# Performance work log

Hardware: AMD Instinct MI355X
Metric: run time of the kernel (lower is better)

Reference implementation:

```python
import jax, jax.numpy as jnp
import numpy as np
import math

B, S, D = 16, 1024, 512

def setup_inputs() -> dict:
    key = jax.random.key(0)
    ks = jax.random.split(key, 7)
    s = 1.0 / math.sqrt(D)
    return {
        "features_4h": jax.random.normal(ks[0], (B, S, D), jnp.float32),
        "features_1d": jax.random.normal(ks[1], (B, S, D), jnp.float32),
        "features_1w": jax.random.normal(ks[2], (B, S, D), jnp.float32),
        "Wq": jax.random.normal(ks[3], (D, D), jnp.float32) * s,
        "bq": jnp.zeros((D,), jnp.float32),
        "Wk": jax.random.normal(ks[4], (D, D), jnp.float32) * s,
        "bk": jnp.zeros((D,), jnp.float32),
        "Wv": jax.random.normal(ks[5], (D, D), jnp.float32) * s,
        "bv": jnp.zeros((D,), jnp.float32),
        "tf_weights": jnp.ones((3,), jnp.float32),
    }

def reference(features_4h, features_1d, features_1w, Wq, bq, Wk, bk, Wv, bv, tf_weights):
    # stacked: [B, T=3, S, D]
    stacked = jnp.stack([features_4h, features_1d, features_1w], axis=1)
    scale = 1.0 / math.sqrt(stacked.shape[-1])
    # torch nn.Linear: x @ W.T + b
    Q = jnp.einsum("btsd,ed->btse", stacked, Wq) + bq
    K = jnp.einsum("btsd,ed->btse", stacked, Wk) + bk
    V = jnp.einsum("btsd,ed->btse", stacked, Wv) + bv
    scores = jnp.einsum("btqd,btkd->btqk", Q, K) * scale  # [B,T,S,S]
    attn = jax.nn.softmax(scores, axis=-1)
    attended = jnp.einsum("btqk,btkd->btqd", attn, V)  # [B,T,S,D]
    w = jax.nn.softmax(tf_weights, axis=0)  # [T]
    return jnp.einsum("btsd,t->bsd", attended, w)  # [B,S,D]
```

## Files before the change

### kernel.cpp

```cpp
#include <hip/hip_runtime.h>
#include <cstdint>

typedef __bf16 bf16x8 __attribute__((ext_vector_type(8)));
typedef unsigned short u16x8 __attribute__((ext_vector_type(8)));
typedef float f32x4 __attribute__((ext_vector_type(4)));


__device__ __forceinline__ unsigned short f2bf(float x){
  unsigned u = __float_as_uint(x);
  u += 0x7fffu + ((u >> 16) & 1u);
  return (unsigned short)(u >> 16);
}

__device__ __forceinline__ void gload16(const void* src, void* dst){
  auto g = reinterpret_cast<const uint32_t __attribute__((address_space(1)))*>(
             reinterpret_cast<uintptr_t>(src));
  auto l = reinterpret_cast<uint32_t __attribute__((address_space(3)))*>(
             reinterpret_cast<uintptr_t>(dst));
  __builtin_amdgcn_global_load_lds(g, l, 16, 0, 0);
}

__device__ __forceinline__ void stage_tile(const unsigned short* __restrict__ g, size_t ld,
                                           unsigned short* l, int tid){
  #pragma unroll
  for (int i = 0; i < 4; ++i){
    int j = i * 256 + tid;
    int r = j >> 3, cc = j & 7;
    int c = cc ^ (r & 7);
    gload16(g + (size_t)r * ld + c * 8, l + (size_t)(i * 256 + (tid & 192)) * 8);
  }
}

__device__ __forceinline__ bf16x8 frag_at(const unsigned short* l, int row, int kch){
  int ch = kch ^ (row & 7);
  return *(const bf16x8*)(l + (row << 6) + (ch << 3));
}

__global__ void k_w1(const float* __restrict__ Wk, const float* __restrict__ bq,
                     float* __restrict__ w1){
  __shared__ float red[4][64];
  int d = blockIdx.x * 64 + (threadIdx.x & 63);
  int eq = threadIdx.x >> 6;
  float s = 0.f;
  #pragma unroll 8
  for (int e = eq * 128; e < eq * 128 + 128; ++e) s += Wk[(size_t)e * 512 + d] * bq[e];
  red[eq][threadIdx.x & 63] = s;
  __syncthreads();
  if (eq == 0)
    w1[d] = (red[0][threadIdx.x] + red[1][threadIdx.x] + red[2][threadIdx.x] +
             red[3][threadIdx.x]) * 0.04419417382415922f;
}

__global__ void k_conv_wt(const float* __restrict__ Wq, const float* __restrict__ Wk,
                          unsigned short* __restrict__ WqT, unsigned short* __restrict__ WkT){
  __shared__ float tl[64][65];
  int bi = blockIdx.x;
  const float* src = (bi & 64) ? Wk : Wq;
  unsigned short* dst = (bi & 64) ? WkT : WqT;
  int te = (bi >> 3) & 7, td = bi & 7;
  int tid = threadIdx.x;
  #pragma unroll
  for (int i = 0; i < 4; ++i){
    int q = i * 256 + tid;
    int r = q >> 4, c4 = q & 15;
    f32x4 v = *(const f32x4*)(src + (size_t)(te * 64 + r) * 512 + td * 64 + c4 * 4);
    tl[r][c4 * 4 + 0] = v[0]; tl[r][c4 * 4 + 1] = v[1];
    tl[r][c4 * 4 + 2] = v[2]; tl[r][c4 * 4 + 3] = v[3];
  }
  __syncthreads();
  #pragma unroll
  for (int i = 0; i < 2; ++i){
    int q = i * 256 + tid;
    int r = q >> 3, c8 = q & 7;
    u16x8 o;
    #pragma unroll
    for (int j = 0; j < 8; ++j) o[j] = f2bf(tl[c8 * 8 + j][r]);
    *(u16x8*)(dst + (size_t)(td * 64 + r) * 512 + te * 64 + c8 * 8) = o;
  }
}

__global__ void k_conv_wv(const float* __restrict__ Wv, unsigned short* __restrict__ out){
  size_t e = ((size_t)blockIdx.x * 256 + threadIdx.x) * 8;
  f32x4 v0 = *(const f32x4*)(Wv + e), v1 = *(const f32x4*)(Wv + e + 4);
  u16x8 o;
  o[0] = f2bf(v0[0]); o[1] = f2bf(v0[1]); o[2] = f2bf(v0[2]); o[3] = f2bf(v0[3]);
  o[4] = f2bf(v1[0]); o[5] = f2bf(v1[1]); o[6] = f2bf(v1[2]); o[7] = f2bf(v1[3]);
  *(u16x8*)(out + e) = o;
}

__global__ void k_conv_feat(const float* __restrict__ f0, const float* __restrict__ f1,
                            const float* __restrict__ f2, const float* __restrict__ w1,
                            unsigned short* __restrict__ Xb, float* __restrict__ vcol){
  size_t i = (size_t)blockIdx.x * blockDim.x + threadIdx.x;
  size_t e = i * 8;
  size_t bt = e >> 19;
  size_t rest = e & ((1u << 19) - 1);
  int b = (int)(bt / 3), t = (int)(bt % 3);
  const float* src = (t == 0 ? f0 : (t == 1 ? f1 : f2)) + ((size_t)b << 19) + rest;
  f32x4 v0 = *(const f32x4*)(src);
  f32x4 v1 = *(const f32x4*)(src + 4);
  u16x8 o;
  o[0] = f2bf(v0[0]); o[1] = f2bf(v0[1]); o[2] = f2bf(v0[2]); o[3] = f2bf(v0[3]);
  o[4] = f2bf(v1[0]); o[5] = f2bf(v1[1]); o[6] = f2bf(v1[2]); o[7] = f2bf(v1[3]);
  *(u16x8*)(Xb + e) = o;
  int l = threadIdx.x & 63;
  f32x4 wa = *(const f32x4*)(w1 + l * 8);
  f32x4 wb = *(const f32x4*)(w1 + l * 8 + 4);
  float p = v0[0]*wa[0] + v0[1]*wa[1] + v0[2]*wa[2] + v0[3]*wa[3]
          + v1[0]*wb[0] + v1[1]*wb[1] + v1[2]*wb[2] + v1[3]*wb[3];
  p += __shfl_xor(p, 1);  p += __shfl_xor(p, 2);  p += __shfl_xor(p, 4);
  p += __shfl_xor(p, 8);  p += __shfl_xor(p, 16); p += __shfl_xor(p, 32);
  if (l == 0) vcol[i >> 6] = p;
}

template<int MODE>
__global__ __launch_bounds__(256, 2)
void k_gemm_proj(const unsigned short* __restrict__ A, const unsigned short* __restrict__ Bm,
                 const float* __restrict__ bias, unsigned short* __restrict__ C, int N, float scale){
  __shared__ __align__(16) unsigned short Al[2][8192];
  __shared__ __align__(16) unsigned short Bl[2][8192];
  const int tid = threadIdx.x;
  const int l  = tid & 63;
  const int wid = tid >> 6;
  const int lr = l & 15;
  const int lg = l >> 4;
  const int cpx = gridDim.x >> 3;
  const int wg = (blockIdx.x & 7) * cpx + (blockIdx.x >> 3);
  const int nbc = N >> 7;
  int rb, cb;
  if (MODE == 1){ cb = wg >> 2; rb = wg & 3; }
  else          { rb = wg / nbc; cb = wg % nbc; }
  const unsigned short* Ab = A + (size_t)rb * 128 * 512;
  const unsigned short* Bb = Bm + (size_t)cb * 128 * 512;

  const f32x4 zero4 = {0.f, 0.f, 0.f, 0.f};
  f32x4 acc[4][4];
  #pragma unroll
  for (int i = 0; i < 4; ++i)
    #pragma unroll
    for (int j = 0; j < 4; ++j) acc[i][j] = zero4;

  stage_tile(Ab, 512, &Al[0][0], tid);
  stage_tile(Bb, 512, &Bl[0][0], tid);
  __syncthreads();

  const int wr = wid >> 1, wc = wid & 1;

  for (int kb = 0; kb < 8; ++kb){
    const int cur = kb & 1;
    if (kb < 7){
      stage_tile(Ab + (kb + 1) * 64, 512, &Al[cur ^ 1][0], tid);
      stage_tile(Bb + (kb + 1) * 64, 512, &Bl[cur ^ 1][0], tid);
    }
    #pragma unroll
    for (int ks = 0; ks < 2; ++ks){
      bf16x8 af[4], bf[4];
      #pragma unroll
      for (int i = 0; i < 4; ++i) af[i] = frag_at(&Al[cur][0], wr * 64 + i * 16 + lr, ks * 4 + lg);
      #pragma unroll
      for (int j = 0; j < 4; ++j) bf[j] = frag_at(&Bl[cur][0], wc * 64 + j * 16 + lr, ks * 4 + lg);
      #pragma unroll
      for (int i = 0; i < 4; ++i)
        #pragma unroll
        for (int j = 0; j < 4; ++j)
          acc[i][j] = __builtin_amdgcn_mfma_f32_16x16x32_bf16(af[i], bf[j], acc[i][j], 0, 0, 0);
    }
    __syncthreads();
  }

  #pragma unroll
  for (int j = 0; j < 4; ++j){
    int col = cb * 128 + wc * 64 + j * 16 + lr;
    float bc = (MODE == 0 && bias) ? bias[col] : 0.f;
    #pragma unroll
    for (int i = 0; i < 4; ++i){
      int row0 = rb * 128 + wr * 64 + i * 16 + lg * 4;
      #pragma unroll
      for (int r = 0; r < 4; ++r){
        int row = row0 + r;
        float v = (acc[i][j][r] + ((MODE == 0) ? bc : bias[row])) * scale;
        size_t addr;
        if (MODE == 0) addr = (size_t)row * N + col;
        else           addr = ((size_t)(col >> 10) << 19) + ((size_t)row << 10) + (size_t)(col & 1023);
        C[addr] = f2bf(v);
      }
    }
  }
}

__global__ __launch_bounds__(256, 2)
void k_gemm_qk(const unsigned short* __restrict__ Gb, const unsigned short* __restrict__ Xb,
               unsigned short* __restrict__ S, int bt0){
  __shared__ __align__(16) unsigned short Al[2][8192];
  __shared__ __align__(16) unsigned short Bl[2][8192];
  const int tid = threadIdx.x;
  const int l  = tid & 63;
  const int wid = tid >> 6;
  const int lr = l & 15;
  const int lg = l >> 4;
  const int cpx = gridDim.x >> 3;
  const int wg = (blockIdx.x & 7) * cpx + (blockIdx.x >> 3);
  const int btl = wg >> 6;
  const int bt = bt0 + btl;
  const int tile = wg & 63;
  const int rb = tile >> 3, cb = tile & 7;
  const unsigned short* Ab = Gb + ((size_t)bt << 19) + (size_t)rb * 128 * 512;
  const unsigned short* Bb = Xb + ((size_t)bt << 19) + (size_t)cb * 128 * 512;
  unsigned short* Cb = S + ((size_t)btl << 20);

  const f32x4 zero4 = {0.f, 0.f, 0.f, 0.f};
  f32x4 acc[4][4];
  #pragma unroll
  for (int i = 0; i < 4; ++i)
    #pragma unroll
    for (int j = 0; j < 4; ++j) acc[i][j] = zero4;

  stage_tile(Ab, 512, &Al[0][0], tid);
  stage_tile(Bb, 512, &Bl[0][0], tid);
  __syncthreads();

  const int wr = wid >> 1, wc = wid & 1;

  for (int kb = 0; kb < 8; ++kb){
    const int cur = kb & 1;
    if (kb < 7){
      stage_tile(Ab + (kb + 1) * 64, 512, &Al[cur ^ 1][0], tid);
      stage_tile(Bb + (kb + 1) * 64, 512, &Bl[cur ^ 1][0], tid);
    }
    #pragma unroll
    for (int ks = 0; ks < 2; ++ks){
      bf16x8 af[4], bf[4];
      #pragma unroll
      for (int i = 0; i < 4; ++i) af[i] = frag_at(&Al[cur][0], wr * 64 + i * 16 + lr, ks * 4 + lg);
      #pragma unroll
      for (int j = 0; j < 4; ++j) bf[j] = frag_at(&Bl[cur][0], wc * 64 + j * 16 + lr, ks * 4 + lg);
      #pragma unroll
      for (int i = 0; i < 4; ++i)
        #pragma unroll
        for (int j = 0; j < 4; ++j)
          acc[i][j] = __builtin_amdgcn_mfma_f32_16x16x32_bf16(af[i], bf[j], acc[i][j], 0, 0, 0);
    }
    __syncthreads();
  }

  #pragma unroll
  for (int j = 0; j < 4; ++j){
    int col = cb * 128 + wc * 64 + j * 16 + lr;
    #pragma unroll
    for (int i = 0; i < 4; ++i){
      int row0 = rb * 128 + wr * 64 + i * 16 + lg * 4;
      #pragma unroll
      for (int r = 0; r < 4; ++r){
        _Float16 h = (_Float16)acc[i][j][r];
        Cb[((size_t)(row0 + r) << 10) + col] = __builtin_bit_cast(unsigned short, h);
      }
    }
  }
}

__global__ __launch_bounds__(256)
void k_softmax(unsigned short* __restrict__ S, const float* __restrict__ vcol,
               const float* __restrict__ tfw, int bt0){
  const int wid = threadIdx.x >> 6, l = threadIdx.x & 63;
  const size_t row = (size_t)blockIdx.x * 4 + wid;
  const int bt = bt0 + (int)(row >> 10);
  const int t = bt % 3;
  float t0 = tfw[0], t1 = tfw[1], t2 = tfw[2];
  float tm = fmaxf(t0, fmaxf(t1, t2));
  float e0 = __expf(t0 - tm), e1 = __expf(t1 - tm), e2 = __expf(t2 - tm);
  float w = (t == 0 ? e0 : (t == 1 ? e1 : e2)) / (e0 + e1 + e2);

  const float* vr = vcol + ((size_t)bt << 10) + l * 16;
  unsigned short* rp = S + (row << 10) + l * 16;
  u16x8 a = *(const u16x8*)rp;
  u16x8 b = *(const u16x8*)(rp + 8);
  f32x4 va0 = *(const f32x4*)(vr), va1 = *(const f32x4*)(vr + 4);
  f32x4 va2 = *(const f32x4*)(vr + 8), va3 = *(const f32x4*)(vr + 12);
  float x[16];
  #pragma unroll
  for (int j = 0; j < 8; ++j){
    x[j]     = (float)__builtin_bit_cast(_Float16, (unsigned short)a[j]);
    x[8 + j] = (float)__builtin_bit_cast(_Float16, (unsigned short)b[j]);
  }
  x[0] += va0[0]; x[1] += va0[1]; x[2]  += va0[2]; x[3]  += va0[3];
  x[4] += va1[0]; x[5] += va1[1]; x[6]  += va1[2]; x[7]  += va1[3];
  x[8] += va2[0]; x[9] += va2[1]; x[10] += va2[2]; x[11] += va2[3];
  x[12]+= va3[0]; x[13]+= va3[1]; x[14] += va3[2]; x[15] += va3[3];
  float m = x[0];
  #pragma unroll
  for (int j = 1; j < 16; ++j) m = fmaxf(m, x[j]);
  m = fmaxf(m, __shfl_xor(m, 1));
  m = fmaxf(m, __shfl_xor(m, 2));
  m = fmaxf(m, __shfl_xor(m, 4));
  m = fmaxf(m, __shfl_xor(m, 8));
  m = fmaxf(m, __shfl_xor(m, 16));
  m = fmaxf(m, __shfl_xor(m, 32));
  float s = 0.f;
  #pragma unroll
  for (int j = 0; j < 16; ++j){ x[j] = __expf(x[j] - m); s += x[j]; }
  s += __shfl_xor(s, 1);
  s += __shfl_xor(s, 2);
  s += __shfl_xor(s, 4);
  s += __shfl_xor(s, 8);
  s += __shfl_xor(s, 16);
  s += __shfl_xor(s, 32);
  float sc = w / s;
  u16x8 oa, ob;
  #pragma unroll
  for (int j = 0; j < 8; ++j){
    oa[j] = f2bf(x[j] * sc);
    ob[j] = f2bf(x[8 + j] * sc);
  }
  *(u16x8*)rp = oa;
  *(u16x8*)(rp + 8) = ob;
}

__global__ __launch_bounds__(256, 2)
void k_gemm_pv(const unsigned short* __restrict__ P, const unsigned short* __restrict__ Vt,
               float* __restrict__ out, int b0){
  __shared__ __align__(16) unsigned short Al[2][8192];
  __shared__ __align__(16) unsigned short Bl[2][8192];
  const int tid = threadIdx.x;
  const int l  = tid & 63;
  const int wid = tid >> 6;
  const int lr = l & 15;
  const int lg = l >> 4;
  const int cpx = gridDim.x >> 3;
  const int wg = (blockIdx.x & 7) * cpx + (blockIdx.x >> 3);
  const int bl = wg >> 5;
  const int b = b0 + bl;
  const int tile = wg & 31;
  const int rb = tile >> 2, cb = tile & 3;

  const f32x4 zero4 = {0.f, 0.f, 0.f, 0.f};
  f32x4 acc[4][4];
  #pragma unroll
  for (int i = 0; i < 4; ++i)
    #pragma unroll
    for (int j = 0; j < 4; ++j) acc[i][j] = zero4;

  {
    const unsigned short* Ab = P  + ((size_t)(bl * 3) << 20) + (size_t)rb * 128 * 1024;
    const unsigned short* Bb = Vt + ((size_t)(b * 3) << 19) + (size_t)cb * 128 * 1024;
    stage_tile(Ab, 1024, &Al[0][0], tid);
    stage_tile(Bb, 1024, &Bl[0][0], tid);
  }
  __syncthreads();

  const int wr = wid >> 1, wc = wid & 1;

  #pragma unroll 2
  for (int kb = 0; kb < 48; ++kb){
    const int cur = kb & 1;
    if (kb < 47){
      int kn = kb + 1;
      int t = kn >> 4, kk = kn & 15;
      const unsigned short* Ab = P  + ((size_t)(bl * 3 + t) << 20) + (size_t)rb * 128 * 1024 + kk * 64;
      const unsigned short* Bb = Vt + ((size_t)(b * 3 + t) << 19) + (size_t)cb * 128 * 1024 + kk * 64;
      stage_tile(Ab, 1024, &Al[cur ^ 1][0], tid);
      stage_tile(Bb, 1024, &Bl[cur ^ 1][0], tid);
    }
    #pragma unroll
    for (int ks = 0; ks < 2; ++ks){
      bf16x8 af[4], bf[4];
      #pragma unroll
      for (int i = 0; i < 4; ++i) af[i] = frag_at(&Al[cur][0], wr * 64 + i * 16 + lr, ks * 4 + lg);
      #pragma unroll
      for (int j = 0; j < 4; ++j) bf[j] = frag_at(&Bl[cur][0], wc * 64 + j * 16 + lr, ks * 4 + lg);
      #pragma unroll
      for (int i = 0; i < 4; ++i)
        #pragma unroll
        for (int j = 0; j < 4; ++j)
          acc[i][j] = __builtin_amdgcn_mfma_f32_16x16x32_bf16(af[i], bf[j], acc[i][j], 0, 0, 0);
    }
    __syncthreads();
  }

  float* ob = out + ((size_t)b << 19);
  #pragma unroll
  for (int j = 0; j < 4; ++j){
    int col = cb * 128 + wc * 64 + j * 16 + lr;
    #pragma unroll
    for (int i = 0; i < 4; ++i){
      int row0 = rb * 128 + wr * 64 + i * 16 + lg * 4;
      #pragma unroll
      for (int r = 0; r < 4; ++r){
        ob[((size_t)(row0 + r) << 9) + col] = acc[i][j][r];
      }
    }
  }
}

extern "C" void kernel_launch(void* const* d_in, const int* in_sizes, int n_in,
                              void* d_out, int out_size, void* d_ws, size_t ws_size,
                              hipStream_t stream){
  (void)in_sizes; (void)n_in; (void)out_size;
  const float* f4h = (const float*)d_in[0];
  const float* f1d = (const float*)d_in[1];
  const float* f1w = (const float*)d_in[2];
  const float* Wq  = (const float*)d_in[3];
  const float* bq  = (const float*)d_in[4];
  const float* Wk  = (const float*)d_in[5];
  const float* bk  = (const float*)d_in[6];
  const float* Wv  = (const float*)d_in[7];
  const float* bv  = (const float*)d_in[8];
  const float* tfw = (const float*)d_in[9];
  (void)bk;
  float* out = (float*)d_out;

  const size_t N48 = (size_t)48 * 1024 * 512;
  unsigned short* Gb  = (unsigned short*)d_ws;
  unsigned short* Xb  = Gb + N48;
  unsigned short* Vt  = Xb + N48;
  float*          vcol = (float*)(Vt + N48);
  unsigned short* WqT = (unsigned short*)(vcol + 49152);
  unsigned short* WkT = WqT + 262144;
  unsigned short* Wv16= WkT + 262144;
  unsigned short* Mt  = Wv16 + 262144;
  unsigned short* Sb  = WqT;

  const float SC = 0.04419417382415922f;
  const size_t base = 3 * N48 * 2 + 49152 * 4;
  const size_t s_full = (size_t)48 * 1024 * 1024 * 2;

  k_w1<<<8, 256, 0, stream>>>(Wk, bq, vcol);
  float* w1 = (float*)(Mt + 262144);
  k_w1<<<8, 256, 0, stream>>>(Wk, bq, w1);
  k_conv_wt<<<128, 256, 0, stream>>>(Wq, Wk, WqT, WkT);
  k_conv_wv<<<128, 256, 0, stream>>>(Wv, Wv16);
  k_conv_feat<<<12288, 256, 0, stream>>>(f4h, f1d, f1w, w1, Xb, vcol);
  k_gemm_proj<0><<<16, 256, 0, stream>>>(WkT, WqT, nullptr, Mt, 512, SC);
  k_gemm_proj<0><<<1536, 256, 0, stream>>>(Xb, Mt, nullptr, Gb, 512, 1.0f);
  k_gemm_proj<1><<<1536, 256, 0, stream>>>(Wv16, Xb, bv, Vt, 49152, 1.0f);

  if (ws_size >= base + 2048 + s_full){
    k_gemm_qk<<<3072, 256, 0, stream>>>(Gb, Xb, Sb, 0);
    k_softmax<<<12288, 256, 0, stream>>>(Sb, vcol, tfw, 0);
    k_gemm_pv<<<512, 256, 0, stream>>>(Sb, Vt, out, 0);
  } else {
    for (int h = 0; h < 2; ++h){
      int bt0 = h * 24;
      k_gemm_qk<<<1536, 256, 0, stream>>>(Gb, Xb, Sb, bt0);
      k_softmax<<<6144, 256, 0, stream>>>(Sb, vcol, tfw, bt0);
      k_gemm_pv<<<256, 256, 0, stream>>>(Sb, Vt, out, h * 8);
    }
  }
}
```

Measured before the change: 273.6 us.

## Replace 128x128 GEMMs with 256x256 eight-wave pipelined MFMA kernel and split-K PV

Replaces the projection, QK and PV GEMM kernels with one templated 512-thread kernel that computes 256x256 output tiles. It uses half-tile staged global-to-LDS loads two k-steps ahead, explicit vmcnt/lgkmcnt waits, sched barriers and setprio around the MFMA bursts. The PV stage is split along K into two halves that accumulate into a memset-zeroed output with fp32 atomics, and a redundant k_w1 launch is dropped. The larger tiles raise data reuse per LDS byte and cut global traffic. In exchange the kernel needs more LDS and registers, has fewer blocks, and adds atomic contention plus a memset.

New measurement: 334.8 us. 1.22x slower.

```diff
diff --git a/kernel.cpp b/kernel.cpp
--- a/kernel.cpp
+++ b/kernel.cpp
@@ -20,6 +20,11 @@
   __builtin_amdgcn_global_load_lds(g, l, 16, 0, 0);
 }
 
+#define SCHED0 __builtin_amdgcn_sched_barrier(0)
+#define SBAR() do { SCHED0; __builtin_amdgcn_s_barrier(); SCHED0; } while (0)
+#define WAITVM(N) do { asm volatile("s_waitcnt vmcnt(" #N ")" ::: "memory"); SCHED0; } while (0)
+#define WAITLGKM0() do { asm volatile("s_waitcnt lgkmcnt(0)" ::: "memory"); SCHED0; } while (0)
+
 __device__ __forceinline__ void stage_tile(const unsigned short* __restrict__ g, size_t ld,
                                            unsigned short* l, int tid){
   #pragma unroll
@@ -28,6 +33,17 @@
     int r = j >> 3, cc = j & 7;
     int c = cc ^ (r & 7);
     gload16(g + (size_t)r * ld + c * 8, l + (size_t)(i * 256 + (tid & 192)) * 8);
+  }
+}
+
+__device__ __forceinline__ void stage_half(const unsigned short* __restrict__ g, int ld,
+                                           unsigned short* l, int tid){
+  #pragma unroll
+  for (int i = 0; i < 2; ++i){
+    int j = i * 512 + tid;
+    int r = j >> 3, cc = j & 7;
+    int c = cc ^ (r & 7);
+    gload16(g + (size_t)r * ld + c * 8, l + (size_t)(i * 512 + (tid & 448)) * 8);
   }
 }
 
@@ -113,10 +129,9 @@
   if (l == 0) vcol[i >> 6] = p;
 }
 
-template<int MODE>
 __global__ __launch_bounds__(256, 2)
-void k_gemm_proj(const unsigned short* __restrict__ A, const unsigned short* __restrict__ Bm,
-                 const float* __restrict__ bias, unsigned short* __restrict__ C, int N, float scale){
+void k_gemm_mt(const unsigned short* __restrict__ A, const unsigned short* __restrict__ Bm,
+               unsigned short* __restrict__ C, float scale){
   __shared__ __align__(16) unsigned short Al[2][8192];
   __shared__ __align__(16) unsigned short Bl[2][8192];
   const int tid = threadIdx.x;
@@ -124,12 +139,7 @@
   const int wid = tid >> 6;
   const int lr = l & 15;
   const int lg = l >> 4;
-  const int cpx = gridDim.x >> 3;
-  const int wg = (blockIdx.x & 7) * cpx + (blockIdx.x >> 3);
-  const int nbc = N >> 7;
-  int rb, cb;
-  if (MODE == 1){ cb = wg >> 2; rb = wg & 3; }
-  else          { rb = wg / nbc; cb = wg % nbc; }
+  const int rb = blockIdx.x >> 2, cb = blockIdx.x & 3;
   const unsigned short* Ab = A + (size_t)rb * 128 * 512;
   const unsigned short* Bb = Bm + (size_t)cb * 128 * 512;
 
@@ -171,91 +181,146 @@
   #pragma unroll
   for (int j = 0; j < 4; ++j){
     int col = cb * 128 + wc * 64 + j * 16 + lr;
-    float bc = (MODE == 0 && bias) ? bias[col] : 0.f;
     #pragma unroll
     for (int i = 0; i < 4; ++i){
       int row0 = rb * 128 + wr * 64 + i * 16 + lg * 4;
       #pragma unroll
-      for (int r = 0; r < 4; ++r){
-        int row = row0 + r;
-        float v = (acc[i][j][r] + ((MODE == 0) ? bc : bias[row])) * scale;
-        size_t addr;
-        if (MODE == 0) addr = (size_t)row * N + col;
-        else           addr = ((size_t)(col >> 10) << 19) + ((size_t)row << 10) + (size_t)(col & 1023);
-        C[addr] = f2bf(v);
-      }
+      for (int r = 0; r < 4; ++r)
+        C[(size_t)(row0 + r) * 512 + col] = f2bf(acc[i][j][r] * scale);
     }
   }
 }
 
-__global__ __launch_bounds__(256, 2)
-void k_gemm_qk(const unsigned short* __restrict__ Gb, const unsigned short* __restrict__ Xb,
-               unsigned short* __restrict__ S, int bt0){
-  __shared__ __align__(16) unsigned short Al[2][8192];
-  __shared__ __align__(16) unsigned short Bl[2][8192];
+template<int MODE>
+__global__ __launch_bounds__(512, 2)
+void k_mm8(const unsigned short* __restrict__ A, const unsigned short* __restrict__ Bm,
+           const float* __restrict__ bias, void* __restrict__ Cv, int bt0){
+  __shared__ __align__(16) unsigned short Asl[2][16384];
+  __shared__ __align__(16) unsigned short Bsl[2][16384];
   const int tid = threadIdx.x;
-  const int l  = tid & 63;
-  const int wid = tid >> 6;
-  const int lr = l & 15;
-  const int lg = l >> 4;
+  const int l = tid & 63, wid = tid >> 6;
+  const int lr = l & 15, lg = l >> 4;
+  const int wr = wid >> 2, wc = wid & 3;
   const int cpx = gridDim.x >> 3;
   const int wg = (blockIdx.x & 7) * cpx + (blockIdx.x >> 3);
-  const int btl = wg >> 6;
-  const int bt = bt0 + btl;
-  const int tile = wg & 63;
-  const int rb = tile >> 3, cb = tile & 7;
-  const unsigned short* Ab = Gb + ((size_t)bt << 19) + (size_t)rb * 128 * 512;
-  const unsigned short* Bb = Xb + ((size_t)bt << 19) + (size_t)cb * 128 * 512;
-  unsigned short* Cb = S + ((size_t)btl << 20);
+
+  int rb, cb, bidx = 0, kh = 0;
+  if (MODE == 0){ rb = wg >> 1; cb = wg & 1; }
+  else if (MODE == 1){ rb = wg & 1; cb = wg >> 1; }
+  else if (MODE == 2){ bidx = wg >> 4; int tl = wg & 15; rb = tl >> 2; cb = tl & 3; }
+  else { bidx = wg >> 4; int sub = wg & 15; kh = sub >> 3; int tl = sub & 7; rb = tl >> 1; cb = tl & 1; }
+
+  const int NT  = (MODE == 3) ? 24 : 8;
+  const int ldA = (MODE == 3) ? 1024 : 512;
+  const int ldB = (MODE == 3) ? 1024 : 512;
+
+  auto aTile = [&](int t) -> const unsigned short* {
+    if (MODE == 0 || MODE == 1) return A + (size_t)rb * 256 * 512 + t * 64;
+    if (MODE == 2) return A + ((size_t)(bt0 + bidx) << 19) + (size_t)rb * 256 * 512 + t * 64;
+    int g = kh * 24 + t; int tt = g >> 4, kk = g & 15;
+    return A + ((size_t)(bidx * 3 + tt) << 20) + (size_t)rb * 256 * 1024 + kk * 64;
+  };
+  auto bTile = [&](int t) -> const unsigned short* {
+    if (MODE == 0 || MODE == 1) return Bm + (size_t)cb * 256 * 512 + t * 64;
+    if (MODE == 2) return Bm + ((size_t)(bt0 + bidx) << 19) + (size_t)cb * 256 * 512 + t * 64;
+    int g = kh * 24 + t; int tt = g >> 4, kk = g & 15;
+    return Bm + ((size_t)((bt0 + bidx) * 3 + tt) << 19) + (size_t)cb * 256 * 1024 + kk * 64;
+  };
 
   const f32x4 zero4 = {0.f, 0.f, 0.f, 0.f};
-  f32x4 acc[4][4];
-  #pragma unroll
-  for (int i = 0; i < 4; ++i)
-    #pragma unroll
-    for (int j = 0; j < 4; ++j) acc[i][j] = zero4;
-
-  stage_tile(Ab, 512, &Al[0][0], tid);
-  stage_tile(Bb, 512, &Bl[0][0], tid);
-  __syncthreads();
-
-  const int wr = wid >> 1, wc = wid & 1;
-
-  for (int kb = 0; kb < 8; ++kb){
-    const int cur = kb & 1;
-    if (kb < 7){
-      stage_tile(Ab + (kb + 1) * 64, 512, &Al[cur ^ 1][0], tid);
-      stage_tile(Bb + (kb + 1) * 64, 512, &Bl[cur ^ 1][0], tid);
-    }
-    #pragma unroll
-    for (int ks = 0; ks < 2; ++ks){
-      bf16x8 af[4], bf[4];
-      #pragma unroll
-      for (int i = 0; i < 4; ++i) af[i] = frag_at(&Al[cur][0], wr * 64 + i * 16 + lr, ks * 4 + lg);
-      #pragma unroll
-      for (int j = 0; j < 4; ++j) bf[j] = frag_at(&Bl[cur][0], wc * 64 + j * 16 + lr, ks * 4 + lg);
-      #pragma unroll
-      for (int i = 0; i < 4; ++i)
+  f32x4 acc[4][2][4];
+  #pragma unroll
+  for (int s = 0; s < 4; ++s)
+    #pragma unroll
+    for (int p = 0; p < 2; ++p)
+      #pragma unroll
+      for (int j = 0; j < 4; ++j) acc[s][p][j] = zero4;
+
+  stage_half(bTile(0),            ldB, &Bsl[0][0],    tid);
+  stage_half(bTile(0) + 128*ldB,  ldB, &Bsl[0][8192], tid);
+  stage_half(aTile(0),            ldA, &Asl[0][0],    tid);
+  stage_half(aTile(0) + 128*ldA,  ldA, &Asl[0][8192], tid);
+  stage_half(bTile(1),            ldB, &Bsl[1][0],    tid);
+  stage_half(bTile(1) + 128*ldB,  ldB, &Bsl[1][8192], tid);
+  stage_half(aTile(1),            ldA, &Asl[1][0],    tid);
+  WAITVM(6);
+  SBAR();
+
+  #pragma unroll 1
+  for (int t = 0; t < NT; ++t){
+    const int st = t & 1;
+    unsigned short* Acur = &Asl[st][0];
+    unsigned short* Bcur = &Bsl[st][0];
+    bf16x8 bfr[4][2];
+    #pragma unroll
+    for (int s = 0; s < 4; ++s){
+      if (s == 0){
         #pragma unroll
         for (int j = 0; j < 4; ++j)
-          acc[i][j] = __builtin_amdgcn_mfma_f32_16x16x32_bf16(af[i], bf[j], acc[i][j], 0, 0, 0);
+          #pragma unroll
+          for (int kk = 0; kk < 2; ++kk)
+            bfr[j][kk] = frag_at(Bcur, wc * 64 + j * 16 + lr, kk * 4 + lg);
+      }
+      bf16x8 afr[2][2];
+      #pragma unroll
+      for (int p = 0; p < 2; ++p)
+        #pragma unroll
+        for (int kk = 0; kk < 2; ++kk)
+          afr[p][kk] = frag_at(Acur, 64 * s + 32 * wr + p * 16 + lr, kk * 4 + lg);
+
+      if (s == 0){
+        if (t + 1 < NT) stage_half(aTile(t + 1) + 128*ldA, ldA, &Asl[(t + 1) & 1][8192], tid);
+      } else if (s == 1){
+        if (t + 2 < NT) stage_half(bTile(t + 2),           ldB, &Bsl[st][0],    tid);
+      } else if (s == 2){
+        if (t + 2 < NT) stage_half(bTile(t + 2) + 128*ldB, ldB, &Bsl[st][8192], tid);
+      } else {
+        if (t + 2 < NT) stage_half(aTile(t + 2),           ldA, &Asl[st][0],    tid);
+        if (t < NT - 2) { WAITVM(6); } else if (t == NT - 2) { WAITVM(0); }
+      }
+
+      SBAR();
+      WAITLGKM0();
+      __builtin_amdgcn_s_setprio(1);
+      #pragma unroll
+      for (int p = 0; p < 2; ++p)
+        #pragma unroll
+        for (int j = 0; j < 4; ++j)
+          #pragma unroll
+          for (int kk = 0; kk < 2; ++kk)
+            acc[s][p][j] = __builtin_amdgcn_mfma_f32_16x16x32_bf16(afr[p][kk], bfr[j][kk], acc[s][p][j], 0, 0, 0);
+      __builtin_amdgcn_s_setprio(0);
+      SBAR();
     }
-    __syncthreads();
-  }
-
-  #pragma unroll
-  for (int j = 0; j < 4; ++j){
-    int col = cb * 128 + wc * 64 + j * 16 + lr;
-    #pragma unroll
-    for (int i = 0; i < 4; ++i){
-      int row0 = rb * 128 + wr * 64 + i * 16 + lg * 4;
-      #pragma unroll
-      for (int r = 0; r < 4; ++r){
-        _Float16 h = (_Float16)acc[i][j][r];
-        Cb[((size_t)(row0 + r) << 10) + col] = __builtin_bit_cast(unsigned short, h);
+  }
+
+  const int row0 = rb * 256 + 32 * wr + lg * 4;
+  const int col0 = cb * 256 + wc * 64 + lr;
+  #pragma unroll
+  for (int s = 0; s < 4; ++s)
+    #pragma unroll
+    for (int p = 0; p < 2; ++p)
+      #pragma unroll
+      for (int j = 0; j < 4; ++j){
+        const int col = col0 + j * 16;
+        #pragma unroll
+        for (int r = 0; r < 4; ++r){
+          const int row = row0 + 64 * s + 16 * p + r;
+          float v = acc[s][p][j][r];
+          if (MODE == 0){
+            ((unsigned short*)Cv)[(size_t)row * 512 + col] = f2bf(v);
+          } else if (MODE == 1){
+            v += bias[row];
+            ((unsigned short*)Cv)[((size_t)(col >> 10) << 19) + ((size_t)row << 10) + (col & 1023)] = f2bf(v);
+          } else if (MODE == 2){
+            _Float16 h = (_Float16)v;
+            ((unsigned short*)Cv)[((size_t)bidx << 20) + ((size_t)row << 10) + col] =
+                __builtin_bit_cast(unsigned short, h);
+          } else {
+            atomicAdd((float*)Cv + (((size_t)(bt0 + bidx)) << 19) + ((size_t)row << 9) + col, v);
+          }
+        }
       }
-    }
-  }
 }
 
 __global__ __launch_bounds__(256)
@@ -313,82 +378,6 @@
   }
   *(u16x8*)rp = oa;
   *(u16x8*)(rp + 8) = ob;
-}
-
-__global__ __launch_bounds__(256, 2)
-void k_gemm_pv(const unsigned short* __restrict__ P, const unsigned short* __restrict__ Vt,
-               float* __restrict__ out, int b0){
-  __shared__ __align__(16) unsigned short Al[2][8192];
-  __shared__ __align__(16) unsigned short Bl[2][8192];
-  const int tid = threadIdx.x;
-  const int l  = tid & 63;
-  const int wid = tid >> 6;
-  const int lr = l & 15;
-  const int lg = l >> 4;
-  const int cpx = gridDim.x >> 3;
-  const int wg = (blockIdx.x & 7) * cpx + (blockIdx.x >> 3);
-  const int bl = wg >> 5;
-  const int b = b0 + bl;
-  const int tile = wg & 31;
-  const int rb = tile >> 2, cb = tile & 3;
-
-  const f32x4 zero4 = {0.f, 0.f, 0.f, 0.f};
-  f32x4 acc[4][4];
-  #pragma unroll
-  for (int i = 0; i < 4; ++i)
-    #pragma unroll
-    for (int j = 0; j < 4; ++j) acc[i][j] = zero4;
-
-  {
-    const unsigned short* Ab = P  + ((size_t)(bl * 3) << 20) + (size_t)rb * 128 * 1024;
-    const unsigned short* Bb = Vt + ((size_t)(b * 3) << 19) + (size_t)cb * 128 * 1024;
-    stage_tile(Ab, 1024, &Al[0][0], tid);
-    stage_tile(Bb, 1024, &Bl[0][0], tid);
-  }
-  __syncthreads();
-
-  const int wr = wid >> 1, wc = wid & 1;
-
-  #pragma unroll 2
-  for (int kb = 0; kb < 48; ++kb){
-    const int cur = kb & 1;
-    if (kb < 47){
-      int kn = kb + 1;
-      int t = kn >> 4, kk = kn & 15;
-      const unsigned short* Ab = P  + ((size_t)(bl * 3 + t) << 20) + (size_t)rb * 128 * 1024 + kk * 64;
-      const unsigned short* Bb = Vt + ((size_t)(b * 3 + t) << 19) + (size_t)cb * 128 * 1024 + kk * 64;
-      stage_tile(Ab, 1024, &Al[cur ^ 1][0], tid);
-      stage_tile(Bb, 1024, &Bl[cur ^ 1][0], tid);
-    }
-    #pragma unroll
-    for (int ks = 0; ks < 2; ++ks){
-      bf16x8 af[4], bf[4];
-      #pragma unroll
-      for (int i = 0; i < 4; ++i) af[i] = frag_at(&Al[cur][0], wr * 64 + i * 16 + lr, ks * 4 + lg);
-      #pragma unroll
-      for (int j = 0; j < 4; ++j) bf[j] = frag_at(&Bl[cur][0], wc * 64 + j * 16 + lr, ks * 4 + lg);
-      #pragma unroll
-      for (int i = 0; i < 4; ++i)
-        #pragma unroll
-        for (int j = 0; j < 4; ++j)
-          acc[i][j] = __builtin_amdgcn_mfma_f32_16x16x32_bf16(af[i], bf[j], acc[i][j], 0, 0, 0);
-    }
-    __syncthreads();
-  }
-
-  float* ob = out + ((size_t)b << 19);
-  #pragma unroll
-  for (int j = 0; j < 4; ++j){
-    int col = cb * 128 + wc * 64 + j * 16 + lr;
-    #pragma unroll
-    for (int i = 0; i < 4; ++i){
-      int row0 = rb * 128 + wr * 64 + i * 16 + lg * 4;
-      #pragma unroll
-      for (int r = 0; r < 4; ++r){
-        ob[((size_t)(row0 + r) << 9) + col] = acc[i][j][r];
-      }
-    }
-  }
 }
 
 extern "C" void kernel_launch(void* const* d_in, const int* in_sizes, int n_in,
@@ -417,32 +406,32 @@
   unsigned short* WkT = WqT + 262144;
   unsigned short* Wv16= WkT + 262144;
   unsigned short* Mt  = Wv16 + 262144;
+  float*          w1  = (float*)(Mt + 262144);
   unsigned short* Sb  = WqT;
 
   const float SC = 0.04419417382415922f;
   const size_t base = 3 * N48 * 2 + 49152 * 4;
   const size_t s_full = (size_t)48 * 1024 * 1024 * 2;
 
-  k_w1<<<8, 256, 0, stream>>>(Wk, bq, vcol);
-  float* w1 = (float*)(Mt + 262144);
   k_w1<<<8, 256, 0, stream>>>(Wk, bq, w1);
   k_conv_wt<<<128, 256, 0, stream>>>(Wq, Wk, WqT, WkT);
   k_conv_wv<<<128, 256, 0, stream>>>(Wv, Wv16);
   k_conv_feat<<<12288, 256, 0, stream>>>(f4h, f1d, f1w, w1, Xb, vcol);
-  k_gemm_proj<0><<<16, 256, 0, stream>>>(WkT, WqT, nullptr, Mt, 512, SC);
-  k_gemm_proj<0><<<1536, 256, 0, stream>>>(Xb, Mt, nullptr, Gb, 512, 1.0f);
-  k_gemm_proj<1><<<1536, 256, 0, stream>>>(Wv16, Xb, bv, Vt, 49152, 1.0f);
+  k_gemm_mt<<<16, 256, 0, stream>>>(WkT, WqT, Mt, SC);
+  k_mm8<0><<<384, 512, 0, stream>>>(Xb, Mt, nullptr, Gb, 0);
+  k_mm8<1><<<384, 512, 0, stream>>>(Wv16, Xb, bv, Vt, 0);
+  hipMemsetAsync(out, 0, (size_t)16 * 1024 * 512 * 4, stream);
 
   if (ws_size >= base + 2048 + s_full){
-    k_gemm_qk<<<3072, 256, 0, stream>>>(Gb, Xb, Sb, 0);
+    k_mm8<2><<<768, 512, 0, stream>>>(Gb, Xb, nullptr, Sb, 0);
     k_softmax<<<12288, 256, 0, stream>>>(Sb, vcol, tfw, 0);
-    k_gemm_pv<<<512, 256, 0, stream>>>(Sb, Vt, out, 0);
+    k_mm8<3><<<256, 512, 0, stream>>>(Sb, Vt, nullptr, out, 0);
   } else {
     for (int h = 0; h < 2; ++h){
       int bt0 = h * 24;
-      k_gemm_qk<<<1536, 256, 0, stream>>>(Gb, Xb, Sb, bt0);
+      k_mm8<2><<<384, 512, 0, stream>>>(Gb, Xb, nullptr, Sb, bt0);
       k_softmax<<<6144, 256, 0, stream>>>(Sb, vcol, tfw, bt0);
-      k_gemm_pv<<<256, 256, 0, stream>>>(Sb, Vt, out, h * 8);
+      k_mm8<3><<<128, 512, 0, stream>>>(Sb, Vt, nullptr, out, h * 8);
     }
   }
 }
```

## Merge weight prep kernels and stage GEMM epilogues through LDS for coalesced stores

Applied to the files above, without the earlier changes.

The three small weight-preparation kernels and the duplicated w1 launch are merged into one k_prep kernel that dispatches on block index, which removes several launches. The projection and QK GEMM epilogues now write the accumulator tile into shared memory first and then copy it out as 16-byte vector stores per row. Previously each lane stored scattered 2-byte values. This is meant to cut uncoalesced global store traffic for the large S and projection outputs, at the cost of an extra LDS round trip and a barrier.

After: 268.7 us. Within noise of the previous version (-1.8%).

```diff
diff --git a/kernel.cpp b/kernel.cpp
--- a/kernel.cpp
+++ b/kernel.cpp
@@ -36,56 +36,53 @@
   return *(const bf16x8*)(l + (row << 6) + (ch << 3));
 }
 
-__global__ void k_w1(const float* __restrict__ Wk, const float* __restrict__ bq,
-                     float* __restrict__ w1){
-  __shared__ float red[4][64];
-  int d = blockIdx.x * 64 + (threadIdx.x & 63);
-  int eq = threadIdx.x >> 6;
-  float s = 0.f;
-  #pragma unroll 8
-  for (int e = eq * 128; e < eq * 128 + 128; ++e) s += Wk[(size_t)e * 512 + d] * bq[e];
-  red[eq][threadIdx.x & 63] = s;
-  __syncthreads();
-  if (eq == 0)
-    w1[d] = (red[0][threadIdx.x] + red[1][threadIdx.x] + red[2][threadIdx.x] +
-             red[3][threadIdx.x]) * 0.04419417382415922f;
-}
-
-__global__ void k_conv_wt(const float* __restrict__ Wq, const float* __restrict__ Wk,
-                          unsigned short* __restrict__ WqT, unsigned short* __restrict__ WkT){
-  __shared__ float tl[64][65];
-  int bi = blockIdx.x;
-  const float* src = (bi & 64) ? Wk : Wq;
-  unsigned short* dst = (bi & 64) ? WkT : WqT;
-  int te = (bi >> 3) & 7, td = bi & 7;
-  int tid = threadIdx.x;
-  #pragma unroll
-  for (int i = 0; i < 4; ++i){
-    int q = i * 256 + tid;
-    int r = q >> 4, c4 = q & 15;
-    f32x4 v = *(const f32x4*)(src + (size_t)(te * 64 + r) * 512 + td * 64 + c4 * 4);
-    tl[r][c4 * 4 + 0] = v[0]; tl[r][c4 * 4 + 1] = v[1];
-    tl[r][c4 * 4 + 2] = v[2]; tl[r][c4 * 4 + 3] = v[3];
-  }
-  __syncthreads();
-  #pragma unroll
-  for (int i = 0; i < 2; ++i){
-    int q = i * 256 + tid;
-    int r = q >> 3, c8 = q & 7;
+__global__ void k_prep(const float* __restrict__ Wq, const float* __restrict__ Wk,
+                       const float* __restrict__ Wv, const float* __restrict__ bq,
+                       unsigned short* __restrict__ WqT, unsigned short* __restrict__ WkT,
+                       unsigned short* __restrict__ Wv16, float* __restrict__ w1){
+  __shared__ float sh[64 * 65];
+  const int bi = blockIdx.x;
+  const int tid = threadIdx.x;
+  if (bi < 128){
+    const float* src = (bi & 64) ? Wk : Wq;
+    unsigned short* dst = (bi & 64) ? WkT : WqT;
+    int te = (bi >> 3) & 7, td = bi & 7;
+    #pragma unroll
+    for (int i = 0; i < 4; ++i){
+      int q = i * 256 + tid;
+      int r = q >> 4, c4 = q & 15;
+      f32x4 v = *(const f32x4*)(src + (size_t)(te * 64 + r) * 512 + td * 64 + c4 * 4);
+      sh[r * 65 + c4 * 4 + 0] = v[0]; sh[r * 65 + c4 * 4 + 1] = v[1];
+      sh[r * 65 + c4 * 4 + 2] = v[2]; sh[r * 65 + c4 * 4 + 3] = v[3];
+    }
+    __syncthreads();
+    #pragma unroll
+    for (int i = 0; i < 2; ++i){
+      int q = i * 256 + tid;
+      int r = q >> 3, c8 = q & 7;
+      u16x8 o;
+      #pragma unroll
+      for (int j = 0; j < 8; ++j) o[j] = f2bf(sh[(c8 * 8 + j) * 65 + r]);
+      *(u16x8*)(dst + (size_t)(td * 64 + r) * 512 + te * 64 + c8 * 8) = o;
+    }
+  } else if (bi < 256){
+    size_t e = ((size_t)(bi - 128) * 256 + tid) * 8;
+    f32x4 v0 = *(const f32x4*)(Wv + e), v1 = *(const f32x4*)(Wv + e + 4);
     u16x8 o;
-    #pragma unroll
-    for (int j = 0; j < 8; ++j) o[j] = f2bf(tl[c8 * 8 + j][r]);
-    *(u16x8*)(dst + (size_t)(td * 64 + r) * 512 + te * 64 + c8 * 8) = o;
-  }
-}
-
-__global__ void k_conv_wv(const float* __restrict__ Wv, unsigned short* __restrict__ out){
-  size_t e = ((size_t)blockIdx.x * 256 + threadIdx.x) * 8;
-  f32x4 v0 = *(const f32x4*)(Wv + e), v1 = *(const f32x4*)(Wv + e + 4);
-  u16x8 o;
-  o[0] = f2bf(v0[0]); o[1] = f2bf(v0[1]); o[2] = f2bf(v0[2]); o[3] = f2bf(v0[3]);
-  o[4] = f2bf(v1[0]); o[5] = f2bf(v1[1]); o[6] = f2bf(v1[2]); o[7] = f2bf(v1[3]);
-  *(u16x8*)(out + e) = o;
+    o[0] = f2bf(v0[0]); o[1] = f2bf(v0[1]); o[2] = f2bf(v0[2]); o[3] = f2bf(v0[3]);
+    o[4] = f2bf(v1[0]); o[5] = f2bf(v1[1]); o[6] = f2bf(v1[2]); o[7] = f2bf(v1[3]);
+    *(u16x8*)(Wv16 + e) = o;
+  } else {
+    int d = (bi - 256) * 64 + (tid & 63);
+    int eq = tid >> 6;
+    float s = 0.f;
+    #pragma unroll 8
+    for (int e = eq * 128; e < eq * 128 + 128; ++e) s += Wk[(size_t)e * 512 + d] * bq[e];
+    sh[eq * 64 + (tid & 63)] = s;
+    __syncthreads();
+    if (eq == 0)
+      w1[d] = (sh[tid] + sh[64 + tid] + sh[128 + tid] + sh[192 + tid]) * 0.04419417382415922f;
+  }
 }
 
 __global__ void k_conv_feat(const float* __restrict__ f0, const float* __restrict__ f1,
@@ -168,22 +165,40 @@
     __syncthreads();
   }
 
+  unsigned short* eL = &Al[0][0];
   #pragma unroll
   for (int j = 0; j < 4; ++j){
-    int col = cb * 128 + wc * 64 + j * 16 + lr;
-    float bc = (MODE == 0 && bias) ? bias[col] : 0.f;
+    int lcol = wc * 64 + j * 16 + lr;
+    float bc = (MODE == 0) ? (bias ? bias[cb * 128 + lcol] : 0.f) : 0.f;
     #pragma unroll
     for (int i = 0; i < 4; ++i){
-      int row0 = rb * 128 + wr * 64 + i * 16 + lg * 4;
+      int lrow0 = wr * 64 + i * 16 + lg * 4;
       #pragma unroll
       for (int r = 0; r < 4; ++r){
-        int row = row0 + r;
-        float v = (acc[i][j][r] + ((MODE == 0) ? bc : bias[row])) * scale;
-        size_t addr;
-        if (MODE == 0) addr = (size_t)row * N + col;
-        else           addr = ((size_t)(col >> 10) << 19) + ((size_t)row << 10) + (size_t)(col & 1023);
-        C[addr] = f2bf(v);
+        float v;
+        if (MODE == 0) v = (acc[i][j][r] + bc) * scale;
+        else           v = acc[i][j][r] + bias[rb * 128 + lrow0 + r];
+        eL[(lrow0 + r) * 128 + lcol] = f2bf(v);
       }
+    }
+  }
+  __syncthreads();
+  if (MODE == 0){
+    #pragma unroll
+    for (int q = 0; q < 8; ++q){
+      int idx = q * 256 + tid;
+      int row = idx >> 4, col = (idx & 15) * 8;
+      *(u16x8*)(&C[(size_t)(rb * 128 + row) * N + cb * 128 + col]) =
+          *(const u16x8*)(&eL[row * 128 + col]);
+    }
+  } else {
+    size_t base = ((size_t)(cb >> 3) << 19) + (size_t)(cb & 7) * 128;
+    #pragma unroll
+    for (int q = 0; q < 8; ++q){
+      int idx = q * 256 + tid;
+      int row = idx >> 4, col = (idx & 15) * 8;
+      *(u16x8*)(&C[base + ((size_t)(rb * 128 + row) << 10) + col]) =
+          *(const u16x8*)(&eL[row * 128 + col]);
     }
   }
 }
@@ -243,18 +258,27 @@
     __syncthreads();
   }
 
+  unsigned short* eL = &Al[0][0];
   #pragma unroll
   for (int j = 0; j < 4; ++j){
-    int col = cb * 128 + wc * 64 + j * 16 + lr;
+    int lcol = wc * 64 + j * 16 + lr;
     #pragma unroll
     for (int i = 0; i < 4; ++i){
-      int row0 = rb * 128 + wr * 64 + i * 16 + lg * 4;
+      int lrow0 = wr * 64 + i * 16 + lg * 4;
       #pragma unroll
       for (int r = 0; r < 4; ++r){
         _Float16 h = (_Float16)acc[i][j][r];
-        Cb[((size_t)(row0 + r) << 10) + col] = __builtin_bit_cast(unsigned short, h);
+        eL[(lrow0 + r) * 128 + lcol] = __builtin_bit_cast(unsigned short, h);
       }
     }
+  }
+  __syncthreads();
+  #pragma unroll
+  for (int q = 0; q < 8; ++q){
+    int idx = q * 256 + tid;
+    int row = idx >> 4, col = (idx & 15) * 8;
+    *(u16x8*)(&Cb[((size_t)(rb * 128 + row) << 10) + cb * 128 + col]) =
+        *(const u16x8*)(&eL[row * 128 + col]);
   }
 }
 
@@ -417,17 +441,14 @@
   unsigned short* WkT = WqT + 262144;
   unsigned short* Wv16= WkT + 262144;
   unsigned short* Mt  = Wv16 + 262144;
+  float*          w1  = (float*)(Mt + 262144);
   unsigned short* Sb  = WqT;
 
   const float SC = 0.04419417382415922f;
   const size_t base = 3 * N48 * 2 + 49152 * 4;
   const size_t s_full = (size_t)48 * 1024 * 1024 * 2;
 
-  k_w1<<<8, 256, 0, stream>>>(Wk, bq, vcol);
-  float* w1 = (float*)(Mt + 262144);
-  k_w1<<<8, 256, 0, stream>>>(Wk, bq, w1);
-  k_conv_wt<<<128, 256, 0, stream>>>(Wq, Wk, WqT, WkT);
-  k_conv_wv<<<128, 256, 0, stream>>>(Wv, Wv16);
+  k_prep<<<264, 256, 0, stream>>>(Wq, Wk, Wv, bq, WqT, WkT, Wv16, w1);
   k_conv_feat<<<12288, 256, 0, stream>>>(f4h, f1d, f1w, w1, Xb, vcol);
   k_gemm_proj<0><<<16, 256, 0, stream>>>(WkT, WqT, nullptr, Mt, 512, SC);
   k_gemm_proj<0><<<1536, 256, 0, stream>>>(Xb, Mt, nullptr, Gb, 512, 1.0f);
```
